# Performance work log

Hardware: AMD Instinct MI355X
Metric: run time of the kernel (lower is better)

Reference implementation:

```python
import jax, jax.numpy as jnp
import numpy as np

D = 2048
H = 16
HD = D // H
FF = 4 * D
EPS = 1e-5


def layernorm(x, scale, shift):
    mean = jnp.mean(x, axis=-1, keepdims=True)
    var = jnp.mean((x - mean) ** 2, axis=-1, keepdims=True)  # unbiased=False
    return scale * (x - mean) / jnp.sqrt(var + EPS) + shift


def setup_inputs() -> dict:
    key = jax.random.key(0)
    ks = jax.random.split(key, 12)
    s = 0.02
    return {
        "x": jax.random.normal(ks[0], (2, 2048, D), dtype=jnp.float32),
        "ln1_scale": jnp.ones((D,), jnp.float32),
        "ln1_shift": jnp.zeros((D,), jnp.float32),
        "wq": jax.random.normal(ks[1], (D, D), jnp.float32) * s,
        "bq": jnp.zeros((D,), jnp.float32),
        "wk": jax.random.normal(ks[2], (D, D), jnp.float32) * s,
        "bk": jnp.zeros((D,), jnp.float32),
        "wv": jax.random.normal(ks[3], (D, D), jnp.float32) * s,
        "bv": jnp.zeros((D,), jnp.float32),
        "wo": jax.random.normal(ks[4], (D, D), jnp.float32) * s,
        "bo": jnp.zeros((D,), jnp.float32),
        "ln2_scale": jnp.ones((D,), jnp.float32),
        "ln2_shift": jnp.zeros((D,), jnp.float32),
        "w1": jax.random.normal(ks[5], (D, FF), jnp.float32) * s,
        "b1": jnp.zeros((FF,), jnp.float32),
        "w2": jax.random.normal(ks[6], (FF, D), jnp.float32) * s,
        "b2": jnp.zeros((D,), jnp.float32),
    }


def block(x, ln1_scale, ln1_shift, wq, bq, wk, bk, wv, bv, wo, bo,
          ln2_scale, ln2_shift, w1, b1, w2, b2):
    B, S, _ = x.shape
    h = layernorm(x, ln1_scale, ln1_shift)
    q = (h @ wq + bq).reshape(B, S, H, HD).transpose(0, 2, 1, 3)  # [B,H,S,hd]
    k = (h @ wk + bk).reshape(B, S, H, HD).transpose(0, 2, 1, 3)
    v = (h @ wv + bv).reshape(B, S, H, HD).transpose(0, 2, 1, 3)
    scores = jnp.einsum("bhqd,bhkd->bhqk", q, k) / jnp.sqrt(jnp.float32(HD))
    causal = jnp.tril(jnp.ones((S, S), dtype=bool))
    scores = jnp.where(causal[None, None], scores, -jnp.inf)
    attn = jax.nn.softmax(scores, axis=-1)
    ctx = jnp.einsum("bhqk,bhkd->bhqd", attn, v)
    ctx = ctx.transpose(0, 2, 1, 3).reshape(B, S, D)
    x = x + (ctx @ wo + bo)
    h2 = layernorm(x, ln2_scale, ln2_shift)
    ffn = jax.nn.gelu(h2 @ w1 + b1, approximate=False) @ w2 + b2
    return x + ffn


def reference(x, ln1_scale, ln1_shift, wq, bq, wk, bk, wv, bv, wo, bo,
              ln2_scale, ln2_shift, w1, b1, w2, b2):
    return block(x, ln1_scale, ln1_shift, wq, bq, wk, bk, wv, bv, wo, bo,
                 ln2_scale, ln2_shift, w1, b1, w2, b2)
```

## Files before the change

kernel.cpp:

```cpp
#include <hip/hip_runtime.h>
#include <hip/hip_bf16.h>
#include <math.h>

namespace {

constexpr int Dm  = 2048;
constexpr int FFm = 8192;
constexpr int SEQ = 2048;
constexpr int HDm = 128;
constexpr int MR  = 4096;
constexpr int QW  = 3 * Dm;

typedef __bf16 bf16_t;
typedef __bf16 bf16x8 __attribute__((ext_vector_type(8)));
typedef float  f32x4  __attribute__((ext_vector_type(4)));

typedef __attribute__((address_space(1))) const void as1_void;
typedef __attribute__((address_space(3))) void as3_void;

__device__ __forceinline__ void gload_lds16(const void* g, void* l) {
  __builtin_amdgcn_global_load_lds((as1_void*)g, (as3_void*)l, 16, 0, 0);
}

__global__ __launch_bounds__(256)
void ln_kernel(const float* __restrict__ x, const float* __restrict__ sc,
               const float* __restrict__ sh, bf16_t* __restrict__ out)
{
  const int row = blockIdx.x;
  const int tid = threadIdx.x;
  const float4* xr = (const float4*)(x + (size_t)row * Dm);
  float4 v0 = xr[tid*2], v1 = xr[tid*2+1];
  float s  = v0.x+v0.y+v0.z+v0.w + v1.x+v1.y+v1.z+v1.w;
  float s2 = v0.x*v0.x+v0.y*v0.y+v0.z*v0.z+v0.w*v0.w
           + v1.x*v1.x+v1.y*v1.y+v1.z*v1.z+v1.w*v1.w;
  #pragma unroll
  for (int off = 32; off; off >>= 1) { s += __shfl_xor(s, off); s2 += __shfl_xor(s2, off); }
  __shared__ float red[8];
  if ((tid & 63) == 0) { red[(tid>>6)*2] = s; red[(tid>>6)*2+1] = s2; }
  __syncthreads();
  s  = red[0]+red[2]+red[4]+red[6];
  s2 = red[1]+red[3]+red[5]+red[7];
  const float mean = s * (1.f/Dm);
  const float var  = fmaxf(s2 * (1.f/Dm) - mean*mean, 0.f);
  const float rstd = rsqrtf(var + 1e-5f);
  const float4* scp = (const float4*)sc;
  const float4* shp = (const float4*)sh;
  float4 sc0 = scp[tid*2], sc1 = scp[tid*2+1];
  float4 sh0 = shp[tid*2], sh1 = shp[tid*2+1];
  __attribute__((aligned(16))) bf16_t ob[8];
  ob[0] = (bf16_t)((v0.x-mean)*rstd*sc0.x + sh0.x);
  ob[1] = (bf16_t)((v0.y-mean)*rstd*sc0.y + sh0.y);
  ob[2] = (bf16_t)((v0.z-mean)*rstd*sc0.z + sh0.z);
  ob[3] = (bf16_t)((v0.w-mean)*rstd*sc0.w + sh0.w);
  ob[4] = (bf16_t)((v1.x-mean)*rstd*sc1.x + sh1.x);
  ob[5] = (bf16_t)((v1.y-mean)*rstd*sc1.y + sh1.y);
  ob[6] = (bf16_t)((v1.z-mean)*rstd*sc1.z + sh1.z);
  ob[7] = (bf16_t)((v1.w-mean)*rstd*sc1.w + sh1.w);
  *(uint4*)(out + (size_t)row*Dm + tid*8) = *(const uint4*)ob;
}

__global__ __launch_bounds__(256)
void wconv4(const float* __restrict__ wq, const float* __restrict__ wk,
            const float* __restrict__ wv, const float* __restrict__ wo,
            bf16_t* __restrict__ dst)
{
  const int z = blockIdx.z;
  const float* W = (z == 0) ? wq : (z == 1) ? wk : (z == 2) ? wv : wo;
  bf16_t* WT = dst + (size_t)z * Dm * Dm;
  __shared__ float tile[32][33];
  const int tx = threadIdx.x & 31, ty = threadIdx.x >> 5;
  const int nb = blockIdx.x * 32, kb = blockIdx.y * 32;
  #pragma unroll
  for (int p = 0; p < 4; ++p)
    tile[ty+8*p][tx] = W[(size_t)(kb+ty+8*p)*Dm + nb + tx];
  __syncthreads();
  #pragma unroll
  for (int p = 0; p < 4; ++p)
    WT[(size_t)(nb+ty+8*p)*Dm + kb + tx] = (bf16_t)tile[tx][ty+8*p];
}

__global__ __launch_bounds__(256)
void wconv_t(const float* __restrict__ W, bf16_t* __restrict__ WT, int K, int N)
{
  __shared__ float tile[32][33];
  const int tx = threadIdx.x & 31, ty = threadIdx.x >> 5;
  const int nb = blockIdx.x * 32, kb = blockIdx.y * 32;
  #pragma unroll
  for (int p = 0; p < 4; ++p)
    tile[ty+8*p][tx] = W[(size_t)(kb+ty+8*p)*N + nb + tx];
  __syncthreads();
  #pragma unroll
  for (int p = 0; p < 4; ++p)
    WT[(size_t)(nb+ty+8*p)*K + kb + tx] = (bf16_t)tile[tx][ty+8*p];
}

__global__ void bias_concat(const float* __restrict__ bq, const float* __restrict__ bk,
                            const float* __restrict__ bv, float* __restrict__ o)
{
  int i = blockIdx.x*256 + threadIdx.x;
  o[i] = bq[i]; o[Dm+i] = bk[i]; o[2*Dm+i] = bv[i];
}

__global__ __launch_bounds__(256)
void vtrans(const bf16_t* __restrict__ qkv, bf16_t* __restrict__ vT)
{
  __shared__ bf16_t tile[32][33];
  const int tx = threadIdx.x & 31, ty = threadIdx.x >> 5;
  const int s0 = blockIdx.x*32, d0 = blockIdx.y*32, bh = blockIdx.z;
  const int b = bh >> 4, h = bh & 15;
  const bf16_t* src = qkv + (size_t)(b*SEQ)*QW + 2*Dm + h*HDm;
  #pragma unroll
  for (int p = 0; p < 4; ++p)
    tile[ty+8*p][tx] = src[(size_t)(s0+ty+8*p)*QW + d0 + tx];
  __syncthreads();
  bf16_t* dst = vT + (size_t)bh*HDm*SEQ;
  #pragma unroll
  for (int p = 0; p < 4; ++p)
    dst[(size_t)(d0+ty+8*p)*SEQ + s0 + tx] = tile[tx][ty+8*p];
}

template<int MODE>
__global__ __launch_bounds__(512, 2)
void gemm8p(const bf16_t* __restrict__ A, const bf16_t* __restrict__ BT,
            const float* __restrict__ bias,
            void* __restrict__ Cout, void* __restrict__ Cout2,
            int Ndim, int Kslice, int Kstride, int gn)
{
  const int gm = (int)gridDim.x / gn;
  const int cm = gm >> 1, cn = gn >> 2;
  const int c = blockIdx.x & 7;
  const int idx = blockIdx.x >> 3;
  const int mi = idx / cn, ni = idx - mi*cn;
  const int m0 = ((c >> 2)*cm + mi) * 256;
  const int n0 = ((c & 3)*cn + ni) * 256;
  const int kOff = blockIdx.y * Kslice;
  const int tid = threadIdx.x;
  const int lane = tid & 63;
  const int w = tid >> 6;
  const int wr = w >> 2, wc = w & 3;
  const int lr = lane & 15, kg = lane >> 4;

  __shared__ __attribute__((aligned(16))) bf16_t lds[65536];

  f32x4 acc[8][4] = {};

  const int r1   = tid >> 3;
  const int blk1 = (tid & 7) ^ (r1 & 7);
  const size_t rowoff = (size_t)64 * Kstride;
  const bf16_t* pA0 = A  + (size_t)(m0 + r1)*Kstride       + kOff + blk1*8;
  const bf16_t* pA1 = A  + (size_t)(m0 + 128 + r1)*Kstride + kOff + blk1*8;
  const bf16_t* pB0 = BT + (size_t)(n0 + r1)*Kstride       + kOff + blk1*8;
  const bf16_t* pB1 = BT + (size_t)(n0 + 128 + r1)*Kstride + kOff + blk1*8;
  bf16_t* const d0 = lds + (size_t)tid*8;

#define STG(p, region) do { \
    gload_lds16((p), d0 + (size_t)(region)*8192); \
    gload_lds16((p) + rowoff, d0 + (size_t)(region)*8192 + 4096); \
    (p) += 64; } while (0)

  auto readA = [&](int buf, int mh, bf16x8* f) {
    #pragma unroll
    for (int ml = 0; ml < 4; ++ml)
      #pragma unroll
      for (int kk = 0; kk < 2; ++kk) {
        const bf16_t* base = lds + (buf*4 + mh)*8192;
        const int row = wr*64 + ml*16 + lr;
        f[ml*2+kk] = *(const bf16x8*)(base + row*64 + (((kk*4+kg) ^ (row&7))*8));
      }
  };
  auto readB = [&](int buf, int nh, bf16x8* f) {
    #pragma unroll
    for (int nl = 0; nl < 2; ++nl)
      #pragma unroll
      for (int kk = 0; kk < 2; ++kk) {
        const bf16_t* base = lds + (buf*4 + 2 + nh)*8192;
        const int row = wc*32 + nl*16 + lr;
        f[nl*2+kk] = *(const bf16x8*)(base + row*64 + (((kk*4+kg) ^ (row&7))*8));
      }
  };
  auto mfma16 = [&](int mh, int nh, const bf16x8* Af, const bf16x8* Bf) {
    __builtin_amdgcn_s_setprio(1);
    #pragma unroll
    for (int ml = 0; ml < 4; ++ml)
      #pragma unroll
      for (int nl = 0; nl < 2; ++nl)
        #pragma unroll
        for (int kk = 0; kk < 2; ++kk)
          acc[mh*4+ml][nh*2+nl] =
            __builtin_amdgcn_mfma_f32_16x16x32_bf16(Af[ml*2+kk], Bf[nl*2+kk],
                                                    acc[mh*4+ml][nh*2+nl], 0, 0, 0);
    __builtin_amdgcn_s_setprio(0);
  };

#define BAR() __builtin_amdgcn_s_barrier()
#define LGKM0() asm volatile("s_waitcnt lgkmcnt(0)")

  bf16x8 Af0[8], Af1[8], Bf0[4], Bf1[4];
  bf16x8 Af0b[8], Af1b[8], Bf0b[4], Bf1b[4];

  STG(pA0, 0); STG(pA1, 1); STG(pB0, 2); STG(pB1, 3);
  STG(pA0, 4); STG(pA1, 5); STG(pB0, 6); STG(pB1, 7);
  asm volatile("s_waitcnt vmcnt(8)" ::: "memory");
  BAR();

  const int NITER = Kslice >> 7;
  for (int j = 0; j < NITER; ++j) {
    const bool s2 = (j + 1 < NITER);

    readA(0, 0, Af0); readB(0, 0, Bf0);
    BAR(); LGKM0(); mfma16(0, 0, Af0, Bf0); BAR();

    readB(0, 1, Bf1);
    if (s2) STG(pA0, 0);
    BAR(); LGKM0(); mfma16(0, 1, Af0, Bf1); BAR();

    readA(0, 1, Af1);
    if (s2) STG(pB0, 2);
    BAR(); LGKM0(); mfma16(1, 1, Af1, Bf1);
    if (s2) asm volatile("s_waitcnt vmcnt(4)" ::: "memory");
    else    asm volatile("s_waitcnt vmcnt(0)" ::: "memory");
    BAR();

    readA(1, 0, Af0b);
    if (s2) { STG(pA1, 1); STG(pB1, 3); }
    BAR(); LGKM0(); mfma16(1, 0, Af1, Bf0); BAR();

    readB(1, 0, Bf0b);
    BAR(); LGKM0(); mfma16(0, 0, Af0b, Bf0b); BAR();

    readB(1, 1, Bf1b);
    if (s2) { STG(pA0, 4); STG(pB0, 6); }
    BAR(); LGKM0(); mfma16(0, 1, Af0b, Bf1b); BAR();

    readA(1, 1, Af1b);
    if (s2) STG(pB1, 7);
    BAR(); LGKM0(); mfma16(1, 1, Af1b, Bf1b); BAR();

    if (s2) STG(pA1, 5);
    BAR(); mfma16(1, 0, Af1b, Bf0b);
    if (s2) asm volatile("s_waitcnt vmcnt(8)" ::: "memory");
    else    asm volatile("s_waitcnt vmcnt(0)" ::: "memory");
    BAR();
  }
#undef STG
#undef BAR
#undef LGKM0

  if constexpr (MODE == 0 || MODE == 1) {
    __syncthreads();
    #pragma unroll
    for (int NF = 0; NF < 4; ++NF) {
      const int col = (NF>>1)*128 + wc*32 + (NF&1)*16 + lr;
      const float bv = bias[n0 + col];
      #pragma unroll
      for (int MF = 0; MF < 8; ++MF) {
        #pragma unroll
        for (int jj = 0; jj < 4; ++jj) {
          float v = acc[MF][NF][jj] + bv;
          if constexpr (MODE == 1) v = 0.5f*v*(1.f + erff(v*0.70710678118f));
          const int row = (MF>>2)*128 + wr*64 + (MF&3)*16 + kg*4 + jj;
          const int adr = row*256 + (((col >> 3) ^ (row & 7)) << 3) + (col & 7);
          lds[adr] = (bf16_t)v;
        }
      }
    }
    __syncthreads();
    bf16_t* outp = (bf16_t*)Cout;
    #pragma unroll
    for (int i = 0; i < 16; ++i) {
      const int s = tid + i*512;
      const int row = s >> 5, ch = s & 31;
      uint4 vv = *(const uint4*)(lds + row*256 + ((ch ^ (row & 7)) << 3));
      *(uint4*)(outp + (size_t)(m0 + row)*Ndim + n0 + ch*8) = vv;
    }
  } else {
    float* pout = (float*)(blockIdx.y ? Cout2 : Cout);
    #pragma unroll
    for (int NF = 0; NF < 4; ++NF) {
      const int col = n0 + (NF>>1)*128 + wc*32 + (NF&1)*16 + lr;
      #pragma unroll
      for (int MF = 0; MF < 8; ++MF) {
        const int rbase = m0 + (MF>>2)*128 + wr*64 + (MF&3)*16 + kg*4;
        #pragma unroll
        for (int jj = 0; jj < 4; ++jj)
          pout[(size_t)(rbase + jj)*Ndim + col] = acc[MF][NF][jj];
      }
    }
  }
}

__global__ __launch_bounds__(256)
void splitk_reduce(const float* __restrict__ p0, const float* __restrict__ p1,
                   const float* __restrict__ bias, const float* __restrict__ resid,
                   float* __restrict__ out, int Ndim)
{
  const size_t e = ((size_t)blockIdx.x*256 + threadIdx.x) * 4;
  float4 a = *(const float4*)(p0 + e);
  float4 b = *(const float4*)(p1 + e);
  float4 r = *(const float4*)(resid + e);
  float4 bv = *(const float4*)(bias + (int)(e & (size_t)(Ndim - 1)));
  float4 o;
  o.x = a.x + b.x + bv.x + r.x;
  o.y = a.y + b.y + bv.y + r.y;
  o.z = a.z + b.z + bv.z + r.z;
  o.w = a.w + b.w + bv.w + r.w;
  *(float4*)(out + e) = o;
}

__global__ __launch_bounds__(256)
void flash_attn4(const bf16_t* __restrict__ qkv, const bf16_t* __restrict__ vT,
                 bf16_t* __restrict__ ctx)
{
  const int bid = blockIdx.x;
  const int bh  = (bid & 7) + 8 * ((bid >> 3) & 3);
  const int pr  = bid >> 5;
  const int b = bh >> 4, h = bh & 15;
  const int tid = threadIdx.x;
  const int lane = tid & 63;
  const int w = tid >> 6;
  const int lr = lane & 15, kg = lane >> 4;

  __shared__ __attribute__((aligned(16))) bf16_t Ks[64*128];
  __shared__ __attribute__((aligned(16))) bf16_t Vs[128*64];
  __shared__ __attribute__((aligned(16))) bf16_t Plds[4*2048];

  const bf16_t* kbase = qkv + (size_t)(b*SEQ)*QW + Dm + h*HDm;
  const bf16_t* vbase = vT + (size_t)bh*HDm*SEQ;
  const float scl = 0.08838834764831845f * 1.44269504089f;

  auto stage = [&](int k0) {
    #pragma unroll
    for (int i = 0; i < 4; ++i) {
      const int s = tid + i*256;
      const int row = s >> 4, sl = s & 15;
      gload_lds16(kbase + (size_t)(k0 + row)*QW + (sl ^ (row & 7))*8, Ks + s*8);
    }
    #pragma unroll
    for (int i = 0; i < 4; ++i) {
      const int s = tid + i*256;
      const int row = s >> 3, sl = s & 7;
      gload_lds16(vbase + (size_t)row*SEQ + k0 + (sl ^ (row & 7))*8, Vs + s*8);
    }
  };

  #pragma unroll 1
  for (int pass = 0; pass < 2; ++pass) {
    const int qi = (pass == 0) ? pr : (15 - pr);
    const int Q0 = qi * 128;
    const int q0w = Q0 + w * 32;

    bf16x8 qf[2][4];
    #pragma unroll
    for (int rt = 0; rt < 2; ++rt) {
      const bf16_t* qb = qkv + (size_t)(b*SEQ + q0w + rt*16 + lr)*QW + h*HDm;
      #pragma unroll
      for (int g = 0; g < 4; ++g)
        qf[rt][g] = *(const bf16x8*)(qb + g*32 + kg*8);
    }

    float mrow[2][4], lsum[2][4];
    f32x4 oacc[2][8];
    #pragma unroll
    for (int rt = 0; rt < 2; ++rt) {
      #pragma unroll
      for (int j = 0; j < 4; ++j) { mrow[rt][j] = -INFINITY; lsum[rt][j] = 0.f; }
      #pragma unroll
      for (int dt = 0; dt < 8; ++dt) oacc[rt][dt] = (f32x4){0.f,0.f,0.f,0.f};
    }

    if (pass) __syncthreads();
    const int nsteps = (Q0 + 128) >> 6;
    stage(0);
    for (int t = 0; t < nsteps; ++t) {
      const int k0 = t * 64;
      __syncthreads();
      if (k0 < q0w + 32) {
        f32x4 sa[2][4];
        #pragma unroll
        for (int rt = 0; rt < 2; ++rt)
          #pragma unroll
          for (int ct = 0; ct < 4; ++ct) sa[rt][ct] = (f32x4){0.f,0.f,0.f,0.f};
        #pragma unroll
        for (int ct = 0; ct < 4; ++ct) {
          const int krow = ct*16 + lr;
          #pragma unroll
          for (int g = 0; g < 4; ++g) {
            bf16x8 kf = *(const bf16x8*)(Ks + krow*128 + ((4*g + kg) ^ (krow & 7))*8);
            sa[0][ct] = __builtin_amdgcn_mfma_f32_16x16x32_bf16(qf[0][g], kf, sa[0][ct], 0, 0, 0);
            sa[1][ct] = __builtin_amdgcn_mfma_f32_16x16x32_bf16(qf[1][g], kf, sa[1][ct], 0, 0, 0);
          }
        }
        #pragma unroll
        for (int rt = 0; rt < 2; ++rt)
          #pragma unroll
          for (int ct = 0; ct < 4; ++ct)
            #pragma unroll
            for (int j = 0; j < 4; ++j) sa[rt][ct][j] *= scl;
        if (k0 + 63 > q0w) {
          #pragma unroll
          for (int ct = 0; ct < 4; ++ct) {
            const int kidx = k0 + ct*16 + lr;
            #pragma unroll
            for (int rt = 0; rt < 2; ++rt)
              #pragma unroll
              for (int j = 0; j < 4; ++j) {
                const int qidx = q0w + rt*16 + kg*4 + j;
                if (kidx > qidx) sa[rt][ct][j] = -INFINITY;
              }
          }
        }
        #pragma unroll
        for (int rt = 0; rt < 2; ++rt) {
          #pragma unroll
          for (int j = 0; j < 4; ++j) {
            const int prow = kg*4 + j;
            float x0 = sa[rt][0][j], x1 = sa[rt][1][j], x2 = sa[rt][2][j], x3 = sa[rt][3][j];
            float v = fmaxf(fmaxf(x0, x1), fmaxf(x2, x3));
            v = fmaxf(v, __shfl_xor(v, 1));
            v = fmaxf(v, __shfl_xor(v, 2));
            v = fmaxf(v, __shfl_xor(v, 4));
            v = fmaxf(v, __shfl_xor(v, 8));
            const float mn = fmaxf(mrow[rt][j], v);
            const float alpha = exp2f(mrow[rt][j] - mn);
            mrow[rt][j] = mn;
            float p0 = exp2f(x0 - mn), p1 = exp2f(x1 - mn);
            float p2 = exp2f(x2 - mn), p3 = exp2f(x3 - mn);
            float ss = (p0 + p1) + (p2 + p3);
            ss += __shfl_xor(ss, 1);
            ss += __shfl_xor(ss, 2);
            ss += __shfl_xor(ss, 4);
            ss += __shfl_xor(ss, 8);
            lsum[rt][j] = lsum[rt][j]*alpha + ss;
            #pragma unroll
            for (int dt = 0; dt < 8; ++dt) oacc[rt][dt][j] *= alpha;
            const int base = w*2048 + rt*1024 + prow*64;
            const int sw = (prow & 7) << 3;
            Plds[(base + ( 0 + lr)) ^ sw] = (bf16_t)p0;
            Plds[(base + (16 + lr)) ^ sw] = (bf16_t)p1;
            Plds[(base + (32 + lr)) ^ sw] = (bf16_t)p2;
            Plds[(base + (48 + lr)) ^ sw] = (bf16_t)p3;
          }
        }
        bf16x8 pf[2][2];
        {
          const int sw = (lr & 7) << 3;
          #pragma unroll
          for (int rt = 0; rt < 2; ++rt) {
            pf[rt][0] = *(const bf16x8*)(Plds + ((w*2048 + rt*1024 + lr*64 +      kg*8) ^ sw));
            pf[rt][1] = *(const bf16x8*)(Plds + ((w*2048 + rt*1024 + lr*64 + 32 + kg*8) ^ sw));
          }
        }
        #pragma unroll
        for (int dt = 0; dt < 8; ++dt) {
          const int vrow = dt*16 + lr;
          #pragma unroll
          for (int kc = 0; kc < 2; ++kc) {
            bf16x8 vf = *(const bf16x8*)(Vs + vrow*64 + ((4*kc + kg) ^ (vrow & 7))*8);
            oacc[0][dt] = __builtin_amdgcn_mfma_f32_16x16x32_bf16(pf[0][kc], vf, oacc[0][dt], 0, 0, 0);
            oacc[1][dt] = __builtin_amdgcn_mfma_f32_16x16x32_bf16(pf[1][kc], vf, oacc[1][dt], 0, 0, 0);
          }
        }
      }
      __syncthreads();
      if (t + 1 < nsteps) stage((t + 1) * 64);
    }

    #pragma unroll
    for (int rt = 0; rt < 2; ++rt) {
      bf16_t* cb = ctx + (size_t)(b*SEQ + q0w + rt*16 + kg*4)*Dm + h*HDm;
      #pragma unroll
      for (int j = 0; j < 4; ++j) {
        const float inv = 1.f / lsum[rt][j];
        #pragma unroll
        for (int dt = 0; dt < 8; ++dt)
          cb[(size_t)j*Dm + dt*16 + lr] = (bf16_t)(oacc[rt][dt][j] * inv);
      }
    }
  }
}

}

extern "C" void kernel_launch(void* const* d_in, const int* in_sizes, int n_in,
                              void* d_out, int out_size, void* d_ws, size_t ws_size,
                              hipStream_t stream)
{
  const float* x   = (const float*)d_in[0];
  const float* g1  = (const float*)d_in[1];
  const float* s1  = (const float*)d_in[2];
  const float* wq  = (const float*)d_in[3];
  const float* bq  = (const float*)d_in[4];
  const float* wk  = (const float*)d_in[5];
  const float* bk  = (const float*)d_in[6];
  const float* wv  = (const float*)d_in[7];
  const float* bv  = (const float*)d_in[8];
  const float* wo  = (const float*)d_in[9];
  const float* bo  = (const float*)d_in[10];
  const float* g2  = (const float*)d_in[11];
  const float* s2  = (const float*)d_in[12];
  const float* w1  = (const float*)d_in[13];
  const float* b1  = (const float*)d_in[14];
  const float* w2  = (const float*)d_in[15];
  const float* b2  = (const float*)d_in[16];
  float* out = (float*)d_out;

  char* p = (char*)d_ws;
  bf16_t* wqkvT = (bf16_t*)p;  p += (size_t)QW*Dm*2;
  bf16_t* woT   = (bf16_t*)p;  p += (size_t)Dm*Dm*2;
  bf16_t* w1T   = (bf16_t*)p;  p += (size_t)FFm*Dm*2;
  bf16_t* w2T   = (bf16_t*)p;  p += (size_t)Dm*FFm*2;
  float*  bqkv  = (float*)p;   p += (size_t)QW*4;
  bf16_t* hbuf  = (bf16_t*)p;  p += (size_t)MR*Dm*2;
  bf16_t* qkv   = (bf16_t*)p;  p += (size_t)MR*QW*2;
  bf16_t* vTb   = (bf16_t*)p;  p += (size_t)32*HDm*SEQ*2;
  bf16_t* ctx   = (bf16_t*)p;  p += (size_t)MR*Dm*2;
  float*  x1    = (float*)p;   p += (size_t)MR*Dm*4;
  bf16_t* ffn1  = qkv;
  float*  prj0  = (float*)qkv;
  float*  prj1  = (float*)qkv + (size_t)MR*Dm;
  float*  f2p0  = (float*)w1T;
  float*  f2p1  = (float*)wqkvT;

  wconv4<<<dim3(Dm/32, Dm/32, 4), 256, 0, stream>>>(wq, wk, wv, wo, wqkvT);
  wconv_t<<<dim3(FFm/32, Dm/32), 256, 0, stream>>>(w1, w1T, Dm, FFm);
  wconv_t<<<dim3(Dm/32, FFm/32), 256, 0, stream>>>(w2, w2T, FFm, Dm);
  bias_concat<<<dim3(Dm/256), 256, 0, stream>>>(bq, bk, bv, bqkv);

  ln_kernel<<<dim3(MR), 256, 0, stream>>>(x, g1, s1, hbuf);
  gemm8p<0><<<dim3((QW/256)*(MR/256), 1), 512, 0, stream>>>(
      hbuf, wqkvT, bqkv, qkv, nullptr, QW, Dm, Dm, QW/256);
  vtrans<<<dim3(SEQ/32, HDm/32, 32), 256, 0, stream>>>(qkv, vTb);
  flash_attn4<<<dim3(256), 256, 0, stream>>>(qkv, vTb, ctx);
  gemm8p<3><<<dim3((Dm/256)*(MR/256), 2), 512, 0, stream>>>(
      ctx, woT, nullptr, prj0, prj1, Dm, Dm/2, Dm, Dm/256);
  splitk_reduce<<<dim3(MR*Dm/1024), 256, 0, stream>>>(prj0, prj1, bo, x, x1, Dm);
  ln_kernel<<<dim3(MR), 256, 0, stream>>>(x1, g2, s2, hbuf);
  gemm8p<1><<<dim3((FFm/256)*(MR/256), 1), 512, 0, stream>>>(
      hbuf, w1T, b1, ffn1, nullptr, FFm, Dm, Dm, FFm/256);
  gemm8p<3><<<dim3((Dm/256)*(MR/256), 2), 512, 0, stream>>>(
      ffn1, w2T, nullptr, f2p0, f2p1, Dm, FFm/2, FFm, Dm/256);
  splitk_reduce<<<dim3(MR*Dm/1024), 256, 0, stream>>>(f2p0, f2p1, b2, x1, out, Dm);
}
```

Baseline: 711.5 us.

## Fuse split-K reduce with second layernorm and give each attention block one query tile

Adds a kernel that sums the two split-K partials, bias and residual, writes x1, and computes the second layernorm in the same pass. This removes one kernel launch and a full re-read of x1. Flash attention no longer pairs two query tiles per block: it launches 512 blocks, one per 128-row query tile, with heavy tiles scheduled first. That gives more parallelism but drops the built-in load balancing between long and short causal rows.

```diff
diff --git a/kernel.cpp b/kernel.cpp
--- a/kernel.cpp
+++ b/kernel.cpp
@@ -60,6 +60,55 @@
 }
 
 __global__ __launch_bounds__(256)
+void ln_fused(const float* __restrict__ p0, const float* __restrict__ p1,
+              const float* __restrict__ bias, const float* __restrict__ resid,
+              const float* __restrict__ sc, const float* __restrict__ sh,
+              float* __restrict__ x1, bf16_t* __restrict__ out)
+{
+  const int row = blockIdx.x;
+  const int tid = threadIdx.x;
+  const size_t base = (size_t)row * Dm + tid*8;
+  float v[8];
+  #pragma unroll
+  for (int hh = 0; hh < 2; ++hh) {
+    float4 a  = *(const float4*)(p0 + base + hh*4);
+    float4 b  = *(const float4*)(p1 + base + hh*4);
+    float4 r  = *(const float4*)(resid + base + hh*4);
+    float4 bv = *(const float4*)(bias + tid*8 + hh*4);
+    v[hh*4+0] = a.x + b.x + bv.x + r.x;
+    v[hh*4+1] = a.y + b.y + bv.y + r.y;
+    v[hh*4+2] = a.z + b.z + bv.z + r.z;
+    v[hh*4+3] = a.w + b.w + bv.w + r.w;
+  }
+  *(float4*)(x1 + base)     = *(const float4*)&v[0];
+  *(float4*)(x1 + base + 4) = *(const float4*)&v[4];
+  float s = 0.f, s2 = 0.f;
+  #pragma unroll
+  for (int j = 0; j < 8; ++j) { s += v[j]; s2 += v[j]*v[j]; }
+  #pragma unroll
+  for (int off = 32; off; off >>= 1) { s += __shfl_xor(s, off); s2 += __shfl_xor(s2, off); }
+  __shared__ float red[8];
+  if ((tid & 63) == 0) { red[(tid>>6)*2] = s; red[(tid>>6)*2+1] = s2; }
+  __syncthreads();
+  s  = red[0]+red[2]+red[4]+red[6];
+  s2 = red[1]+red[3]+red[5]+red[7];
+  const float mean = s * (1.f/Dm);
+  const float var  = fmaxf(s2 * (1.f/Dm) - mean*mean, 0.f);
+  const float rstd = rsqrtf(var + 1e-5f);
+  __attribute__((aligned(16))) bf16_t ob[8];
+  #pragma unroll
+  for (int hh = 0; hh < 2; ++hh) {
+    float4 scv = *(const float4*)(sc + tid*8 + hh*4);
+    float4 shv = *(const float4*)(sh + tid*8 + hh*4);
+    ob[hh*4+0] = (bf16_t)((v[hh*4+0]-mean)*rstd*scv.x + shv.x);
+    ob[hh*4+1] = (bf16_t)((v[hh*4+1]-mean)*rstd*scv.y + shv.y);
+    ob[hh*4+2] = (bf16_t)((v[hh*4+2]-mean)*rstd*scv.z + shv.z);
+    ob[hh*4+3] = (bf16_t)((v[hh*4+3]-mean)*rstd*scv.w + shv.w);
+  }
+  *(uint4*)(out + base) = *(const uint4*)ob;
+}
+
+__global__ __launch_bounds__(256)
 void wconv4(const float* __restrict__ wq, const float* __restrict__ wk,
             const float* __restrict__ wv, const float* __restrict__ wo,
             bf16_t* __restrict__ dst)
@@ -308,17 +357,19 @@
 }
 
 __global__ __launch_bounds__(256)
-void flash_attn4(const bf16_t* __restrict__ qkv, const bf16_t* __restrict__ vT,
+void flash_attn6(const bf16_t* __restrict__ qkv, const bf16_t* __restrict__ vT,
                  bf16_t* __restrict__ ctx)
 {
   const int bid = blockIdx.x;
   const int bh  = (bid & 7) + 8 * ((bid >> 3) & 3);
-  const int pr  = bid >> 5;
+  const int qi  = 15 - (bid >> 5);
   const int b = bh >> 4, h = bh & 15;
+  const int Q0 = qi * 128;
   const int tid = threadIdx.x;
   const int lane = tid & 63;
   const int w = tid >> 6;
   const int lr = lane & 15, kg = lane >> 4;
+  const int q0w = Q0 + w * 32;
 
   __shared__ __attribute__((aligned(16))) bf16_t Ks[64*128];
   __shared__ __attribute__((aligned(16))) bf16_t Vs[128*64];
@@ -343,138 +394,130 @@
     }
   };
 
-  #pragma unroll 1
-  for (int pass = 0; pass < 2; ++pass) {
-    const int qi = (pass == 0) ? pr : (15 - pr);
-    const int Q0 = qi * 128;
-    const int q0w = Q0 + w * 32;
-
-    bf16x8 qf[2][4];
-    #pragma unroll
-    for (int rt = 0; rt < 2; ++rt) {
-      const bf16_t* qb = qkv + (size_t)(b*SEQ + q0w + rt*16 + lr)*QW + h*HDm;
-      #pragma unroll
-      for (int g = 0; g < 4; ++g)
-        qf[rt][g] = *(const bf16x8*)(qb + g*32 + kg*8);
-    }
-
-    float mrow[2][4], lsum[2][4];
-    f32x4 oacc[2][8];
-    #pragma unroll
-    for (int rt = 0; rt < 2; ++rt) {
-      #pragma unroll
-      for (int j = 0; j < 4; ++j) { mrow[rt][j] = -INFINITY; lsum[rt][j] = 0.f; }
-      #pragma unroll
-      for (int dt = 0; dt < 8; ++dt) oacc[rt][dt] = (f32x4){0.f,0.f,0.f,0.f};
-    }
-
-    if (pass) __syncthreads();
-    const int nsteps = (Q0 + 128) >> 6;
-    stage(0);
-    for (int t = 0; t < nsteps; ++t) {
-      const int k0 = t * 64;
-      __syncthreads();
-      if (k0 < q0w + 32) {
-        f32x4 sa[2][4];
-        #pragma unroll
-        for (int rt = 0; rt < 2; ++rt)
+  bf16x8 qf[2][4];
+  #pragma unroll
+  for (int rt = 0; rt < 2; ++rt) {
+    const bf16_t* qb = qkv + (size_t)(b*SEQ + q0w + rt*16 + lr)*QW + h*HDm;
+    #pragma unroll
+    for (int g = 0; g < 4; ++g)
+      qf[rt][g] = *(const bf16x8*)(qb + g*32 + kg*8);
+  }
+
+  float mrow[2][4], lsum[2][4];
+  f32x4 oacc[2][8];
+  #pragma unroll
+  for (int rt = 0; rt < 2; ++rt) {
+    #pragma unroll
+    for (int j = 0; j < 4; ++j) { mrow[rt][j] = -INFINITY; lsum[rt][j] = 0.f; }
+    #pragma unroll
+    for (int dt = 0; dt < 8; ++dt) oacc[rt][dt] = (f32x4){0.f,0.f,0.f,0.f};
+  }
+
+  const int nsteps = (Q0 + 128) >> 6;
+  stage(0);
+  for (int t = 0; t < nsteps; ++t) {
+    const int k0 = t * 64;
+    __syncthreads();
+    if (k0 < q0w + 32) {
+      f32x4 sa[2][4];
+      #pragma unroll
+      for (int rt = 0; rt < 2; ++rt)
+        #pragma unroll
+        for (int ct = 0; ct < 4; ++ct) sa[rt][ct] = (f32x4){0.f,0.f,0.f,0.f};
+      #pragma unroll
+      for (int ct = 0; ct < 4; ++ct) {
+        const int krow = ct*16 + lr;
+        #pragma unroll
+        for (int g = 0; g < 4; ++g) {
+          bf16x8 kf = *(const bf16x8*)(Ks + krow*128 + ((4*g + kg) ^ (krow & 7))*8);
+          sa[0][ct] = __builtin_amdgcn_mfma_f32_16x16x32_bf16(qf[0][g], kf, sa[0][ct], 0, 0, 0);
+          sa[1][ct] = __builtin_amdgcn_mfma_f32_16x16x32_bf16(qf[1][g], kf, sa[1][ct], 0, 0, 0);
+        }
+      }
+      #pragma unroll
+      for (int rt = 0; rt < 2; ++rt)
+        #pragma unroll
+        for (int ct = 0; ct < 4; ++ct)
           #pragma unroll
-          for (int ct = 0; ct < 4; ++ct) sa[rt][ct] = (f32x4){0.f,0.f,0.f,0.f};
+          for (int j = 0; j < 4; ++j) sa[rt][ct][j] *= scl;
+      if (k0 + 63 > q0w) {
         #pragma unroll
         for (int ct = 0; ct < 4; ++ct) {
-          const int krow = ct*16 + lr;
+          const int kidx = k0 + ct*16 + lr;
           #pragma unroll
-          for (int g = 0; g < 4; ++g) {
-            bf16x8 kf = *(const bf16x8*)(Ks + krow*128 + ((4*g + kg) ^ (krow & 7))*8);
-            sa[0][ct] = __builtin_amdgcn_mfma_f32_16x16x32_bf16(qf[0][g], kf, sa[0][ct], 0, 0, 0);
-            sa[1][ct] = __builtin_amdgcn_mfma_f32_16x16x32_bf16(qf[1][g], kf, sa[1][ct], 0, 0, 0);
-          }
+          for (int rt = 0; rt < 2; ++rt)
+            #pragma unroll
+            for (int j = 0; j < 4; ++j) {
+              const int qidx = q0w + rt*16 + kg*4 + j;
+              if (kidx > qidx) sa[rt][ct][j] = -INFINITY;
+            }
         }
-        #pragma unroll
-        for (int rt = 0; rt < 2; ++rt)
+      }
+      #pragma unroll
+      for (int rt = 0; rt < 2; ++rt) {
+        #pragma unroll
+        for (int j = 0; j < 4; ++j) {
+          const int prow = kg*4 + j;
+          float x0 = sa[rt][0][j], x1 = sa[rt][1][j], x2 = sa[rt][2][j], x3 = sa[rt][3][j];
+          float v = fmaxf(fmaxf(x0, x1), fmaxf(x2, x3));
+          v = fmaxf(v, __shfl_xor(v, 1));
+          v = fmaxf(v, __shfl_xor(v, 2));
+          v = fmaxf(v, __shfl_xor(v, 4));
+          v = fmaxf(v, __shfl_xor(v, 8));
+          const float mn = fmaxf(mrow[rt][j], v);
+          const float alpha = exp2f(mrow[rt][j] - mn);
+          mrow[rt][j] = mn;
+          float p0 = exp2f(x0 - mn), p1 = exp2f(x1 - mn);
+          float p2 = exp2f(x2 - mn), p3 = exp2f(x3 - mn);
+          float ss = (p0 + p1) + (p2 + p3);
+          ss += __shfl_xor(ss, 1);
+          ss += __shfl_xor(ss, 2);
+          ss += __shfl_xor(ss, 4);
+          ss += __shfl_xor(ss, 8);
+          lsum[rt][j] = lsum[rt][j]*alpha + ss;
           #pragma unroll
-          for (int ct = 0; ct < 4; ++ct)
-            #pragma unroll
-            for (int j = 0; j < 4; ++j) sa[rt][ct][j] *= scl;
-        if (k0 + 63 > q0w) {
-          #pragma unroll
-          for (int ct = 0; ct < 4; ++ct) {
-            const int kidx = k0 + ct*16 + lr;
-            #pragma unroll
-            for (int rt = 0; rt < 2; ++rt)
-              #pragma unroll
-              for (int j = 0; j < 4; ++j) {
-                const int qidx = q0w + rt*16 + kg*4 + j;
-                if (kidx > qidx) sa[rt][ct][j] = -INFINITY;
-              }
-          }
+          for (int dt = 0; dt < 8; ++dt) oacc[rt][dt][j] *= alpha;
+          const int base = w*2048 + rt*1024 + prow*64;
+          const int sw = (prow & 7) << 3;
+          Plds[(base + ( 0 + lr)) ^ sw] = (bf16_t)p0;
+          Plds[(base + (16 + lr)) ^ sw] = (bf16_t)p1;
+          Plds[(base + (32 + lr)) ^ sw] = (bf16_t)p2;
+          Plds[(base + (48 + lr)) ^ sw] = (bf16_t)p3;
         }
+      }
+      bf16x8 pf[2][2];
+      {
+        const int sw = (lr & 7) << 3;
         #pragma unroll
         for (int rt = 0; rt < 2; ++rt) {
-          #pragma unroll
-          for (int j = 0; j < 4; ++j) {
-            const int prow = kg*4 + j;
-            float x0 = sa[rt][0][j], x1 = sa[rt][1][j], x2 = sa[rt][2][j], x3 = sa[rt][3][j];
-            float v = fmaxf(fmaxf(x0, x1), fmaxf(x2, x3));
-            v = fmaxf(v, __shfl_xor(v, 1));
-            v = fmaxf(v, __shfl_xor(v, 2));
-            v = fmaxf(v, __shfl_xor(v, 4));
-            v = fmaxf(v, __shfl_xor(v, 8));
-            const float mn = fmaxf(mrow[rt][j], v);
-            const float alpha = exp2f(mrow[rt][j] - mn);
-            mrow[rt][j] = mn;
-            float p0 = exp2f(x0 - mn), p1 = exp2f(x1 - mn);
-            float p2 = exp2f(x2 - mn), p3 = exp2f(x3 - mn);
-            float ss = (p0 + p1) + (p2 + p3);
-            ss += __shfl_xor(ss, 1);
-            ss += __shfl_xor(ss, 2);
-            ss += __shfl_xor(ss, 4);
-            ss += __shfl_xor(ss, 8);
-            lsum[rt][j] = lsum[rt][j]*alpha + ss;
-            #pragma unroll
-            for (int dt = 0; dt < 8; ++dt) oacc[rt][dt][j] *= alpha;
-            const int base = w*2048 + rt*1024 + prow*64;
-            const int sw = (prow & 7) << 3;
-            Plds[(base + ( 0 + lr)) ^ sw] = (bf16_t)p0;
-            Plds[(base + (16 + lr)) ^ sw] = (bf16_t)p1;
-            Plds[(base + (32 + lr)) ^ sw] = (bf16_t)p2;
-            Plds[(base + (48 + lr)) ^ sw] = (bf16_t)p3;
-          }
+          pf[rt][0] = *(const bf16x8*)(Plds + ((w*2048 + rt*1024 + lr*64 +      kg*8) ^ sw));
+          pf[rt][1] = *(const bf16x8*)(Plds + ((w*2048 + rt*1024 + lr*64 + 32 + kg*8) ^ sw));
         }
-        bf16x8 pf[2][2];
-        {
-          const int sw = (lr & 7) << 3;
-          #pragma unroll
-          for (int rt = 0; rt < 2; ++rt) {
-            pf[rt][0] = *(const bf16x8*)(Plds + ((w*2048 + rt*1024 + lr*64 +      kg*8) ^ sw));
-            pf[rt][1] = *(const bf16x8*)(Plds + ((w*2048 + rt*1024 + lr*64 + 32 + kg*8) ^ sw));
-          }
+      }
+      #pragma unroll
+      for (int dt = 0; dt < 8; ++dt) {
+        const int vrow = dt*16 + lr;
+        #pragma unroll
+        for (int kc = 0; kc < 2; ++kc) {
+          bf16x8 vf = *(const bf16x8*)(Vs + vrow*64 + ((4*kc + kg) ^ (vrow & 7))*8);
+          oacc[0][dt] = __builtin_amdgcn_mfma_f32_16x16x32_bf16(pf[0][kc], vf, oacc[0][dt], 0, 0, 0);
+          oacc[1][dt] = __builtin_amdgcn_mfma_f32_16x16x32_bf16(pf[1][kc], vf, oacc[1][dt], 0, 0, 0);
         }
-        #pragma unroll
-        for (int dt = 0; dt < 8; ++dt) {
-          const int vrow = dt*16 + lr;
-          #pragma unroll
-          for (int kc = 0; kc < 2; ++kc) {
-            bf16x8 vf = *(const bf16x8*)(Vs + vrow*64 + ((4*kc + kg) ^ (vrow & 7))*8);
-            oacc[0][dt] = __builtin_amdgcn_mfma_f32_16x16x32_bf16(pf[0][kc], vf, oacc[0][dt], 0, 0, 0);
-            oacc[1][dt] = __builtin_amdgcn_mfma_f32_16x16x32_bf16(pf[1][kc], vf, oacc[1][dt], 0, 0, 0);
-          }
-        }
-      }
-      __syncthreads();
-      if (t + 1 < nsteps) stage((t + 1) * 64);
-    }
-
-    #pragma unroll
-    for (int rt = 0; rt < 2; ++rt) {
-      bf16_t* cb = ctx + (size_t)(b*SEQ + q0w + rt*16 + kg*4)*Dm + h*HDm;
-      #pragma unroll
-      for (int j = 0; j < 4; ++j) {
-        const float inv = 1.f / lsum[rt][j];
-        #pragma unroll
-        for (int dt = 0; dt < 8; ++dt)
-          cb[(size_t)j*Dm + dt*16 + lr] = (bf16_t)(oacc[rt][dt][j] * inv);
-      }
+      }
+    }
+    __syncthreads();
+    if (t + 1 < nsteps) stage((t + 1) * 64);
+  }
+
+  #pragma unroll
+  for (int rt = 0; rt < 2; ++rt) {
+    bf16_t* cb = ctx + (size_t)(b*SEQ + q0w + rt*16 + kg*4)*Dm + h*HDm;
+    #pragma unroll
+    for (int j = 0; j < 4; ++j) {
+      const float inv = 1.f / lsum[rt][j];
+      #pragma unroll
+      for (int dt = 0; dt < 8; ++dt)
+        cb[(size_t)j*Dm + dt*16 + lr] = (bf16_t)(oacc[rt][dt][j] * inv);
     }
   }
 }
@@ -530,11 +573,10 @@
   gemm8p<0><<<dim3((QW/256)*(MR/256), 1), 512, 0, stream>>>(
       hbuf, wqkvT, bqkv, qkv, nullptr, QW, Dm, Dm, QW/256);
   vtrans<<<dim3(SEQ/32, HDm/32, 32), 256, 0, stream>>>(qkv, vTb);
-  flash_attn4<<<dim3(256), 256, 0, stream>>>(qkv, vTb, ctx);
+  flash_attn6<<<dim3(512), 256, 0, stream>>>(qkv, vTb, ctx);
   gemm8p<3><<<dim3((Dm/256)*(MR/256), 2), 512, 0, stream>>>(
       ctx, woT, nullptr, prj0, prj1, Dm, Dm/2, Dm, Dm/256);
-  splitk_reduce<<<dim3(MR*Dm/1024), 256, 0, stream>>>(prj0, prj1, bo, x, x1, Dm);
-  ln_kernel<<<dim3(MR), 256, 0, stream>>>(x1, g2, s2, hbuf);
+  ln_fused<<<dim3(MR), 256, 0, stream>>>(prj0, prj1, bo, x, g2, s2, x1, hbuf);
   gemm8p<1><<<dim3((FFm/256)*(MR/256), 1), 512, 0, stream>>>(
       hbuf, w1T, b1, ffn1, nullptr, FFm, Dm, Dm, FFm/256);
   gemm8p<3><<<dim3((Dm/256)*(MR/256), 2), 512, 0, stream>>>(
```

Measured after the change: 707.0 us. No clear change (-0.6%).
